# Performance work log

Measured on AMD Instinct MI355X. Metric: run time of the kernel, lower is better.

The kernel has to match this reference:

```python
import jax, jax.numpy as jnp
import numpy as np

N_HEADS = 12


def setup_inputs() -> dict:
    key = jax.random.key(0)
    ks = jax.random.split(key, 4)
    B, S, D = 2, 2048, 768
    x = jax.random.normal(ks[0], (B, S, D), dtype=jnp.float32)
    # nn.Linear-style init scale ~ 1/sqrt(D) to keep logits reasonable
    scale = 1.0 / np.sqrt(D)
    Wq = jax.random.normal(ks[1], (D, D), dtype=jnp.float32) * scale
    Wk = jax.random.normal(ks[2], (D, D), dtype=jnp.float32) * scale
    Wv = jax.random.normal(ks[3], (D, D), dtype=jnp.float32) * scale
    bq = jnp.zeros((D,), jnp.float32)
    bk = jnp.zeros((D,), jnp.float32)
    bv = jnp.zeros((D,), jnp.float32)
    mask = jnp.ones((B, S), jnp.int32)
    return {"x": x, "Wq": Wq, "bq": bq, "Wk": Wk, "bk": bk,
            "Wv": Wv, "bv": bv, "mask": mask}


def reference(x, Wq, bq, Wk, bk, Wv, bv, mask):
    B, S, D = x.shape
    H = N_HEADS
    W = D // H
    # q,k,v: (B,S,D) -> (B,H,S,W)
    def proj(Wm, bm):
        return (x @ Wm.T + bm).reshape(B, S, H, W).transpose(0, 2, 1, 3)
    q, k, v = proj(Wq, bq), proj(Wk, bk), proj(Wv, bv)
    scores = jnp.einsum("bhsw,bhtw->bhst", q, k) / jnp.sqrt(
        jnp.asarray(W, x.dtype))
    # mask: (B,S) -> broadcast over query positions; 0 -> -1e20
    scores = jnp.where(mask[:, None, None, :] == 0,
                       jnp.asarray(-1e20, scores.dtype), scores)
    attn = jax.nn.softmax(scores, axis=-1)  # (B,H,S,S)
    # dropout p=0.0 (eval) -> identity
    ctx = jnp.einsum("bhst,bhtw->bhsw", attn, v)
    hidden = ctx.transpose(0, 2, 1, 3).reshape(B, S, D)
    return hidden
```

## Files before the change

### kernel.cpp

```cpp
#include <hip/hip_runtime.h>
#include <hip/hip_bf16.h>
#include <stdint.h>


typedef __attribute__((ext_vector_type(8))) short bf16x8;
typedef __attribute__((ext_vector_type(4))) float f32x4;
typedef __attribute__((ext_vector_type(8))) unsigned short u16x8;

#define MFMA16(a, b, c) __builtin_amdgcn_mfma_f32_16x16x32_bf16((a), (b), (c), 0, 0, 0)
#define SWZ(row, colb) ((colb) ^ (((row) & 7) << 4))

__device__ __forceinline__ void gl_lds16(const void* g, void* l) {
  __builtin_amdgcn_global_load_lds(
      (__attribute__((address_space(1))) void*)const_cast<void*>(g),
      (__attribute__((address_space(3))) void*)l, 16, 0, 0);
}

__device__ __forceinline__ unsigned short f2bf(float x) {
  unsigned int v = __float_as_uint(x);
  return (unsigned short)((v + 0x7fffu + ((v >> 16) & 1u)) >> 16);
}

__global__ __launch_bounds__(256) void cvt_all(
    const float* __restrict__ x, const float* __restrict__ wq,
    const float* __restrict__ wk, const float* __restrict__ wv,
    unsigned short* __restrict__ xb, unsigned short* __restrict__ wb) {
  int i = blockIdx.x * 256 + threadIdx.x;
  const float* s;
  unsigned short* d;
  int off;
  if (i < 393216)      { s = x;  d = xb;            off = i; }
  else if (i < 466944) { s = wq; d = wb;            off = i - 393216; }
  else if (i < 540672) { s = wk; d = wb + 589824;   off = i - 466944; }
  else                 { s = wv; d = wb + 1179648;  off = i - 540672; }
  const float4* sp = (const float4*)s + (size_t)off * 2;
  float4 a = sp[0], b2 = sp[1];
  u16x8 o;
  o[0] = f2bf(a.x); o[1] = f2bf(a.y); o[2] = f2bf(a.z); o[3] = f2bf(a.w);
  o[4] = f2bf(b2.x); o[5] = f2bf(b2.y); o[6] = f2bf(b2.z); o[7] = f2bf(b2.w);
  *((u16x8*)d + off) = o;
}

__global__ __launch_bounds__(256) void proj_gemm(
    const unsigned short* __restrict__ xb, const unsigned short* __restrict__ wb,
    const float* __restrict__ bq, const float* __restrict__ bk, const float* __restrict__ bv,
    unsigned short* __restrict__ qw, unsigned short* __restrict__ kw,
    unsigned short* __restrict__ vw) {
  __shared__ unsigned short lA[128 * 64];
  __shared__ unsigned short lB[128 * 64];
  const int t = threadIdx.x, lane = t & 63, wave = t >> 6;
  const int wr = wave >> 1, wc = wave & 1;
  const int mbase = blockIdx.x * 128;
  const int wsel = blockIdx.y / 6;
  const int nbase = (blockIdx.y % 6) * 128;
  const unsigned short* wmat = wb + (size_t)wsel * 589824;

  f32x4 acc[4][4];
#pragma unroll
  for (int i = 0; i < 4; i++)
#pragma unroll
    for (int j = 0; j < 4; j++) acc[i][j] = (f32x4){0.f, 0.f, 0.f, 0.f};

  char* lAc = (char*)lA;
  char* lBc = (char*)lB;

  for (int kt = 0; kt < 768; kt += 64) {
#pragma unroll
    for (int i = 0; i < 4; i++) {
      int p = t * 16 + i * 4096;
      int row = p >> 7, colb = p & 127;
      int scol = SWZ(row, colb);
      gl_lds16((const char*)xb + ((size_t)(mbase + row) * 768 + kt) * 2 + scol, lAc + p);
      gl_lds16((const char*)wmat + ((size_t)(nbase + row) * 768 + kt) * 2 + scol, lBc + p);
    }
    __syncthreads();

    bf16x8 af[2][4], bff[2][4];
#pragma unroll
    for (int mf = 0; mf < 4; mf++) {
      int row = wr * 64 + mf * 16 + (lane & 15);
#pragma unroll
      for (int kk = 0; kk < 2; kk++)
        af[kk][mf] = *(const bf16x8*)(lAc + row * 128 + SWZ(row, kk * 64 + (lane >> 4) * 16));
    }
#pragma unroll
    for (int nf = 0; nf < 4; nf++) {
      int row = wc * 64 + nf * 16 + (lane & 15);
#pragma unroll
      for (int kk = 0; kk < 2; kk++)
        bff[kk][nf] = *(const bf16x8*)(lBc + row * 128 + SWZ(row, kk * 64 + (lane >> 4) * 16));
    }
#pragma unroll
    for (int kk = 0; kk < 2; kk++)
#pragma unroll
      for (int mf = 0; mf < 4; mf++)
#pragma unroll
        for (int nf = 0; nf < 4; nf++)
          acc[mf][nf] = MFMA16(af[kk][mf], bff[kk][nf], acc[mf][nf]);
    __syncthreads();
  }

  const float* bias = (wsel == 0) ? bq : ((wsel == 1) ? bk : bv);
  const float QSCALE = 0.125f * 1.44269504089f;
#pragma unroll
  for (int nf = 0; nf < 4; nf++) {
    int n = nbase + wc * 64 + nf * 16 + (lane & 15);
    float bv_ = bias[n];
    int h = n >> 6, wcol = n & 63;
#pragma unroll
    for (int mf = 0; mf < 4; mf++) {
#pragma unroll
      for (int r = 0; r < 4; r++) {
        int m = mbase + wr * 64 + mf * 16 + (lane >> 4) * 4 + r;
        int b = m >> 11, s = m & 2047;
        float val = acc[mf][nf][r] + bv_;
        size_t bh = (size_t)b * 12 + h;
        if (wsel == 0)
          qw[(bh * 2048 + s) * 64 + wcol] = f2bf(val * QSCALE);
        else if (wsel == 1)
          kw[(bh * 2048 + s) * 64 + wcol] = f2bf(val);
        else
          vw[(bh * 64 + wcol) * 2048 + s] = f2bf(val);
      }
    }
  }
}

__global__ __launch_bounds__(256) void attn_kernel(
    const unsigned short* __restrict__ qw, const unsigned short* __restrict__ kw,
    const unsigned short* __restrict__ vw, const int* __restrict__ mask,
    float* __restrict__ out) {
  __shared__ unsigned short lK[2][64 * 64];
  __shared__ unsigned short lV[2][64 * 64];
  __shared__ unsigned short lP[4][16 * 64];
  __shared__ unsigned long long lBal[32];
  const int t = threadIdx.x, lane = t & 63, wave = t >> 6;
  const int hi = lane >> 4, lo = lane & 15;
  const int qb = blockIdx.x, bh = blockIdx.y;
  const int b = bh / 12, h = bh - b * 12;
  char* lPc = (char*)&lP[wave][0];

  {
    const int* mb = mask + (size_t)b * 2048 + t * 8;
    int4 a0 = *(const int4*)mb;
    int4 a1 = *(const int4*)(mb + 4);
    unsigned by = (unsigned)(a0.x != 0) | ((unsigned)(a0.y != 0) << 1) |
                  ((unsigned)(a0.z != 0) << 2) | ((unsigned)(a0.w != 0) << 3) |
                  ((unsigned)(a1.x != 0) << 4) | ((unsigned)(a1.y != 0) << 5) |
                  ((unsigned)(a1.z != 0) << 6) | ((unsigned)(a1.w != 0) << 7);
    ((unsigned char*)lBal)[t] = (unsigned char)by;
  }

  bf16x8 qa0, qa1;
  {
    int qrow = qb * 64 + wave * 16 + lo;
    const char* qp = (const char*)qw + ((size_t)bh * 2048 + qrow) * 128 + hi * 16;
    qa0 = *(const bf16x8*)qp;
    qa1 = *(const bf16x8*)(qp + 64);
  }

  const char* kbaseg = (const char*)kw + (size_t)bh * 262144;
  const char* vbaseg = (const char*)vw + (size_t)bh * 262144;

  const int p0 = t * 16, p1 = t * 16 + 4096;
  const int r0 = p0 >> 7, s0 = SWZ(r0, p0 & 127);
  const int r1 = p1 >> 7, s1 = SWZ(r1, p1 & 127);

#define STAGE(IT, BUF)                                                              \
  do {                                                                              \
    int it_ = (IT);                                                                 \
    gl_lds16(kbaseg + (size_t)it_ * 8192 + r0 * 128 + s0, (char*)lK[(BUF)] + p0);   \
    gl_lds16(vbaseg + (size_t)r0 * 4096 + it_ * 128 + s0, (char*)lV[(BUF)] + p0);   \
    gl_lds16(kbaseg + (size_t)it_ * 8192 + r1 * 128 + s1, (char*)lK[(BUF)] + p1);   \
    gl_lds16(vbaseg + (size_t)r1 * 4096 + it_ * 128 + s1, (char*)lV[(BUF)] + p1);   \
  } while (0)

  f32x4 oacc[4];
#pragma unroll
  for (int nf = 0; nf < 4; nf++) oacc[nf] = (f32x4){0.f, 0.f, 0.f, 0.f};
  float lacc = 0.f;

  STAGE(0, 0);
  __syncthreads();

  for (int it = 0; it < 32; ++it) {
    STAGE((it + 1) & 31, (it + 1) & 1);
    asm volatile("s_waitcnt vmcnt(4)" ::: "memory");
    __builtin_amdgcn_s_barrier();

    const char* lKc = (const char*)lK[it & 1];
    const char* lVc = (const char*)lV[it & 1];

    f32x4 sc[4];
    __builtin_amdgcn_s_setprio(1);
#pragma unroll
    for (int nf = 0; nf < 4; nf++) {
      int row = nf * 16 + lo;
      bf16x8 kb0 = *(const bf16x8*)(lKc + row * 128 + SWZ(row, hi * 16));
      bf16x8 kb1 = *(const bf16x8*)(lKc + row * 128 + SWZ(row, 64 + hi * 16));
      f32x4 z = (f32x4){0.f, 0.f, 0.f, 0.f};
      z = MFMA16(kb0, qa0, z);
      sc[nf] = MFMA16(kb1, qa1, z);
    }
    __builtin_amdgcn_s_setprio(0);

    unsigned long long bal = lBal[it];
    if (bal != ~0ull) {
#pragma unroll
      for (int nf = 0; nf < 4; nf++)
#pragma unroll
        for (int r = 0; r < 4; r++) {
          int key = nf * 16 + hi * 4 + r;
          if (!((bal >> key) & 1)) sc[nf][r] = -30000.f;
        }
    }

#pragma unroll
    for (int nf = 0; nf < 4; nf++) {
      float e0, e1, e2, e3;
      asm("v_exp_f32 %0, %1" : "=v"(e0) : "v"(sc[nf][0]));
      asm("v_exp_f32 %0, %1" : "=v"(e1) : "v"(sc[nf][1]));
      asm("v_exp_f32 %0, %1" : "=v"(e2) : "v"(sc[nf][2]));
      asm("v_exp_f32 %0, %1" : "=v"(e3) : "v"(sc[nf][3]));
      lacc += (e0 + e1) + (e2 + e3);
      unsigned pkA, pkB;
      asm("v_cvt_pk_bf16_f32 %0, %1, %2" : "=v"(pkA) : "v"(e0), "v"(e1));
      asm("v_cvt_pk_bf16_f32 %0, %1, %2" : "=v"(pkB) : "v"(e2), "v"(e3));
      uint2 pk2;
      pk2.x = pkA;
      pk2.y = pkB;
      *(uint2*)(lPc + lo * 128 + SWZ(lo, nf * 32 + hi * 8)) = pk2;
    }

    bf16x8 pa0 = *(const bf16x8*)(lPc + lo * 128 + SWZ(lo, hi * 16));
    bf16x8 pa1 = *(const bf16x8*)(lPc + lo * 128 + SWZ(lo, 64 + hi * 16));
    __builtin_amdgcn_s_setprio(1);
#pragma unroll
    for (int nf = 0; nf < 4; nf++) {
      int row = nf * 16 + lo;
      bf16x8 vb0 = *(const bf16x8*)(lVc + row * 128 + SWZ(row, hi * 16));
      bf16x8 vb1 = *(const bf16x8*)(lVc + row * 128 + SWZ(row, 64 + hi * 16));
      oacc[nf] = MFMA16(pa0, vb0, oacc[nf]);
      oacc[nf] = MFMA16(pa1, vb1, oacc[nf]);
    }
    __builtin_amdgcn_s_setprio(0);
    __builtin_amdgcn_s_barrier();
  }
  asm volatile("s_waitcnt vmcnt(0)" ::: "memory");

  lacc += __shfl_xor(lacc, 16);
  lacc += __shfl_xor(lacc, 32);
#pragma unroll
  for (int r = 0; r < 4; r++) {
    int q = hi * 4 + r;
    float linv = 1.0f / __shfl(lacc, q);
    int s = qb * 64 + wave * 16 + q;
    float* op = out + ((size_t)b * 2048 + s) * 768 + h * 64;
#pragma unroll
    for (int nf = 0; nf < 4; nf++) op[nf * 16 + lo] = oacc[nf][r] * linv;
  }
#undef STAGE
}

extern "C" void kernel_launch(void* const* d_in, const int* in_sizes, int n_in,
                              void* d_out, int out_size, void* d_ws, size_t ws_size,
                              hipStream_t stream) {
  (void)in_sizes; (void)n_in; (void)out_size; (void)ws_size;
  const float* x  = (const float*)d_in[0];
  const float* Wq = (const float*)d_in[1];
  const float* bq = (const float*)d_in[2];
  const float* Wk = (const float*)d_in[3];
  const float* bk = (const float*)d_in[4];
  const float* Wv = (const float*)d_in[5];
  const float* bv = (const float*)d_in[6];
  const int* mask = (const int*)d_in[7];
  float* out = (float*)d_out;

  char* ws = (char*)d_ws;
  unsigned short* xb = (unsigned short*)(ws);
  unsigned short* wb = (unsigned short*)(ws + 6291456);
  unsigned short* qw = (unsigned short*)(ws + 9830400);
  unsigned short* kw = (unsigned short*)(ws + 16121856);
  unsigned short* vw = (unsigned short*)(ws + 22413312);

  cvt_all<<<2400, 256, 0, stream>>>(x, Wq, Wk, Wv, xb, wb);
  proj_gemm<<<dim3(32, 18), 256, 0, stream>>>(xb, wb, bq, bk, bv, qw, kw, vw);
  attn_kernel<<<dim3(32, 24), 256, 0, stream>>>(qw, kw, vw, mask, out);
}
```

Baseline: 94.69 us.

## Switch attention to 32x32 MFMA with key-split waves and register P transpose

Rewrites the attention inner loop to use 32x32x16 bf16 MFMAs, splitting each 64x64 tile across waves as 2 query-halves times 2 key-halves. Softmax probabilities are moved into A-operand layout with v_permlane32_swap instead of a round trip through LDS. Partial outputs and row sums from the two key-halves are reduced through shared memory at the end. The V projection epilogue is also transposed so that V stores are contiguous along the sequence. The change adds a final cross-wave reduction and sync, and sets launch bounds for 4 blocks per CU.

```diff
diff --git a/kernel.cpp b/kernel.cpp
--- a/kernel.cpp
+++ b/kernel.cpp
@@ -5,10 +5,17 @@
 
 typedef __attribute__((ext_vector_type(8))) short bf16x8;
 typedef __attribute__((ext_vector_type(4))) float f32x4;
+typedef __attribute__((ext_vector_type(16))) float f32x16;
 typedef __attribute__((ext_vector_type(8))) unsigned short u16x8;
 
 #define MFMA16(a, b, c) __builtin_amdgcn_mfma_f32_16x16x32_bf16((a), (b), (c), 0, 0, 0)
+#define MFMA32(a, b, c) __builtin_amdgcn_mfma_f32_32x32x16_bf16((a), (b), (c), 0, 0, 0)
 #define SWZ(row, colb) ((colb) ^ (((row) & 7) << 4))
+
+union U32x4BF {
+  unsigned u[4];
+  bf16x8 v;
+};
 
 __device__ __forceinline__ void gl_lds16(const void* g, void* l) {
   __builtin_amdgcn_global_load_lds(
@@ -90,55 +97,78 @@
       for (int kk = 0; kk < 2; kk++)
         bff[kk][nf] = *(const bf16x8*)(lBc + row * 128 + SWZ(row, kk * 64 + (lane >> 4) * 16));
     }
-#pragma unroll
-    for (int kk = 0; kk < 2; kk++)
-#pragma unroll
-      for (int mf = 0; mf < 4; mf++)
-#pragma unroll
-        for (int nf = 0; nf < 4; nf++)
-          acc[mf][nf] = MFMA16(af[kk][mf], bff[kk][nf], acc[mf][nf]);
+    if (wsel == 2) {
+#pragma unroll
+      for (int kk = 0; kk < 2; kk++)
+#pragma unroll
+        for (int mf = 0; mf < 4; mf++)
+#pragma unroll
+          for (int nf = 0; nf < 4; nf++)
+            acc[mf][nf] = MFMA16(bff[kk][nf], af[kk][mf], acc[mf][nf]);
+    } else {
+#pragma unroll
+      for (int kk = 0; kk < 2; kk++)
+#pragma unroll
+        for (int mf = 0; mf < 4; mf++)
+#pragma unroll
+          for (int nf = 0; nf < 4; nf++)
+            acc[mf][nf] = MFMA16(af[kk][mf], bff[kk][nf], acc[mf][nf]);
+    }
     __syncthreads();
   }
 
-  const float* bias = (wsel == 0) ? bq : ((wsel == 1) ? bk : bv);
   const float QSCALE = 0.125f * 1.44269504089f;
-#pragma unroll
-  for (int nf = 0; nf < 4; nf++) {
-    int n = nbase + wc * 64 + nf * 16 + (lane & 15);
-    float bv_ = bias[n];
-    int h = n >> 6, wcol = n & 63;
-#pragma unroll
-    for (int mf = 0; mf < 4; mf++) {
-#pragma unroll
-      for (int r = 0; r < 4; r++) {
-        int m = mbase + wr * 64 + mf * 16 + (lane >> 4) * 4 + r;
-        int b = m >> 11, s = m & 2047;
-        float val = acc[mf][nf][r] + bv_;
-        size_t bh = (size_t)b * 12 + h;
-        if (wsel == 0)
-          qw[(bh * 2048 + s) * 64 + wcol] = f2bf(val * QSCALE);
-        else if (wsel == 1)
-          kw[(bh * 2048 + s) * 64 + wcol] = f2bf(val);
-        else
-          vw[(bh * 64 + wcol) * 2048 + s] = f2bf(val);
-      }
-    }
-  }
-}
-
-__global__ __launch_bounds__(256) void attn_kernel(
+  if (wsel == 2) {
+#pragma unroll
+    for (int nf = 0; nf < 4; nf++) {
+#pragma unroll
+      for (int mf = 0; mf < 4; mf++) {
+#pragma unroll
+        for (int r = 0; r < 4; r++) {
+          int n = nbase + wc * 64 + nf * 16 + (lane >> 4) * 4 + r;
+          int m = mbase + wr * 64 + mf * 16 + (lane & 15);
+          int b_ = m >> 11, s = m & 2047;
+          int h = n >> 6, wcol = n & 63;
+          float val = acc[mf][nf][r] + bv[n];
+          vw[(((size_t)b_ * 12 + h) * 64 + wcol) * 2048 + s] = f2bf(val);
+        }
+      }
+    }
+  } else {
+    const float* bias = (wsel == 0) ? bq : bk;
+#pragma unroll
+    for (int nf = 0; nf < 4; nf++) {
+      int n = nbase + wc * 64 + nf * 16 + (lane & 15);
+      float bv_ = bias[n];
+      int h = n >> 6, wcol = n & 63;
+#pragma unroll
+      for (int mf = 0; mf < 4; mf++) {
+#pragma unroll
+        for (int r = 0; r < 4; r++) {
+          int m = mbase + wr * 64 + mf * 16 + (lane >> 4) * 4 + r;
+          int b_ = m >> 11, s = m & 2047;
+          float val = acc[mf][nf][r] + bv_;
+          size_t bhh = (size_t)b_ * 12 + h;
+          if (wsel == 0)
+            qw[(bhh * 2048 + s) * 64 + wcol] = f2bf(val * QSCALE);
+          else
+            kw[(bhh * 2048 + s) * 64 + wcol] = f2bf(val);
+        }
+      }
+    }
+  }
+}
+
+__global__ __launch_bounds__(256, 4) void attn_kernel(
     const unsigned short* __restrict__ qw, const unsigned short* __restrict__ kw,
     const unsigned short* __restrict__ vw, const int* __restrict__ mask,
     float* __restrict__ out) {
-  __shared__ unsigned short lK[2][64 * 64];
-  __shared__ unsigned short lV[2][64 * 64];
-  __shared__ unsigned short lP[4][16 * 64];
-  __shared__ unsigned long long lBal[32];
+  __shared__ __align__(16) char smem[33536];
   const int t = threadIdx.x, lane = t & 63, wave = t >> 6;
-  const int hi = lane >> 4, lo = lane & 15;
+  const int wq = wave >> 1, wk = wave & 1;
+  const int l31 = lane & 31, hl = lane >> 5;
   const int qb = blockIdx.x, bh = blockIdx.y;
-  const int b = bh / 12, h = bh - b * 12;
-  char* lPc = (char*)&lP[wave][0];
+  const int b = bh / 12, hh = bh - b * 12;
 
   {
     const int* mb = mask + (size_t)b * 2048 + t * 8;
@@ -148,15 +178,15 @@
                   ((unsigned)(a0.z != 0) << 2) | ((unsigned)(a0.w != 0) << 3) |
                   ((unsigned)(a1.x != 0) << 4) | ((unsigned)(a1.y != 0) << 5) |
                   ((unsigned)(a1.z != 0) << 6) | ((unsigned)(a1.w != 0) << 7);
-    ((unsigned char*)lBal)[t] = (unsigned char)by;
-  }
-
-  bf16x8 qa0, qa1;
+    smem[32768 + t] = (char)by;
+  }
+
+  bf16x8 qv[4];
   {
-    int qrow = qb * 64 + wave * 16 + lo;
-    const char* qp = (const char*)qw + ((size_t)bh * 2048 + qrow) * 128 + hi * 16;
-    qa0 = *(const bf16x8*)qp;
-    qa1 = *(const bf16x8*)(qp + 64);
+    int qrow = qb * 64 + wq * 32 + l31;
+    const char* qp = (const char*)qw + ((size_t)bh * 2048 + qrow) * 128 + hl * 16;
+#pragma unroll
+    for (int s = 0; s < 4; s++) qv[s] = *(const bf16x8*)(qp + s * 32);
   }
 
   const char* kbaseg = (const char*)kw + (size_t)bh * 262144;
@@ -166,98 +196,136 @@
   const int r0 = p0 >> 7, s0 = SWZ(r0, p0 & 127);
   const int r1 = p1 >> 7, s1 = SWZ(r1, p1 & 127);
 
-#define STAGE(IT, BUF)                                                              \
-  do {                                                                              \
-    int it_ = (IT);                                                                 \
-    gl_lds16(kbaseg + (size_t)it_ * 8192 + r0 * 128 + s0, (char*)lK[(BUF)] + p0);   \
-    gl_lds16(vbaseg + (size_t)r0 * 4096 + it_ * 128 + s0, (char*)lV[(BUF)] + p0);   \
-    gl_lds16(kbaseg + (size_t)it_ * 8192 + r1 * 128 + s1, (char*)lK[(BUF)] + p1);   \
-    gl_lds16(vbaseg + (size_t)r1 * 4096 + it_ * 128 + s1, (char*)lV[(BUF)] + p1);   \
+#define STAGE(IT, BUF)                                                                   \
+  do {                                                                                   \
+    int it_ = (IT);                                                                      \
+    gl_lds16(kbaseg + (size_t)it_ * 8192 + r0 * 128 + s0, smem + (BUF) * 8192 + p0);     \
+    gl_lds16(vbaseg + (size_t)r0 * 4096 + it_ * 128 + s0, smem + 16384 + (BUF) * 8192 + p0); \
+    gl_lds16(kbaseg + (size_t)it_ * 8192 + r1 * 128 + s1, smem + (BUF) * 8192 + p1);     \
+    gl_lds16(vbaseg + (size_t)r1 * 4096 + it_ * 128 + s1, smem + 16384 + (BUF) * 8192 + p1); \
   } while (0)
 
-  f32x4 oacc[4];
-#pragma unroll
-  for (int nf = 0; nf < 4; nf++) oacc[nf] = (f32x4){0.f, 0.f, 0.f, 0.f};
+  f32x16 oacc[2];
+#pragma unroll
+  for (int wh = 0; wh < 2; wh++)
+#pragma unroll
+    for (int g = 0; g < 16; g++) oacc[wh][g] = 0.f;
   float lacc = 0.f;
 
   STAGE(0, 0);
   __syncthreads();
 
   for (int it = 0; it < 32; ++it) {
-    STAGE((it + 1) & 31, (it + 1) & 1);
-    asm volatile("s_waitcnt vmcnt(4)" ::: "memory");
+    if (it < 31) {
+      STAGE(it + 1, (it + 1) & 1);
+      asm volatile("s_waitcnt vmcnt(4)" ::: "memory");
+    } else {
+      asm volatile("s_waitcnt vmcnt(0)" ::: "memory");
+    }
     __builtin_amdgcn_s_barrier();
 
-    const char* lKc = (const char*)lK[it & 1];
-    const char* lVc = (const char*)lV[it & 1];
-
-    f32x4 sc[4];
+    const char* lKc = smem + (it & 1) * 8192;
+    const char* lVc = smem + 16384 + (it & 1) * 8192;
+
+    f32x16 sc;
+#pragma unroll
+    for (int g = 0; g < 16; g++) sc[g] = 0.f;
+    const int krow = wk * 32 + l31;
     __builtin_amdgcn_s_setprio(1);
 #pragma unroll
-    for (int nf = 0; nf < 4; nf++) {
-      int row = nf * 16 + lo;
-      bf16x8 kb0 = *(const bf16x8*)(lKc + row * 128 + SWZ(row, hi * 16));
-      bf16x8 kb1 = *(const bf16x8*)(lKc + row * 128 + SWZ(row, 64 + hi * 16));
-      f32x4 z = (f32x4){0.f, 0.f, 0.f, 0.f};
-      z = MFMA16(kb0, qa0, z);
-      sc[nf] = MFMA16(kb1, qa1, z);
+    for (int s = 0; s < 4; s++) {
+      bf16x8 kf = *(const bf16x8*)(lKc + krow * 128 + SWZ(krow, s * 32 + hl * 16));
+      sc = MFMA32(kf, qv[s], sc);
     }
     __builtin_amdgcn_s_setprio(0);
 
-    unsigned long long bal = lBal[it];
+    unsigned long long bal = *(const unsigned long long*)(smem + 32768 + it * 8);
     if (bal != ~0ull) {
 #pragma unroll
-      for (int nf = 0; nf < 4; nf++)
-#pragma unroll
-        for (int r = 0; r < 4; r++) {
-          int key = nf * 16 + hi * 4 + r;
-          if (!((bal >> key) & 1)) sc[nf][r] = -30000.f;
-        }
-    }
-
-#pragma unroll
-    for (int nf = 0; nf < 4; nf++) {
-      float e0, e1, e2, e3;
-      asm("v_exp_f32 %0, %1" : "=v"(e0) : "v"(sc[nf][0]));
-      asm("v_exp_f32 %0, %1" : "=v"(e1) : "v"(sc[nf][1]));
-      asm("v_exp_f32 %0, %1" : "=v"(e2) : "v"(sc[nf][2]));
-      asm("v_exp_f32 %0, %1" : "=v"(e3) : "v"(sc[nf][3]));
-      lacc += (e0 + e1) + (e2 + e3);
-      unsigned pkA, pkB;
-      asm("v_cvt_pk_bf16_f32 %0, %1, %2" : "=v"(pkA) : "v"(e0), "v"(e1));
-      asm("v_cvt_pk_bf16_f32 %0, %1, %2" : "=v"(pkB) : "v"(e2), "v"(e3));
-      uint2 pk2;
-      pk2.x = pkA;
-      pk2.y = pkB;
-      *(uint2*)(lPc + lo * 128 + SWZ(lo, nf * 32 + hi * 8)) = pk2;
-    }
-
-    bf16x8 pa0 = *(const bf16x8*)(lPc + lo * 128 + SWZ(lo, hi * 16));
-    bf16x8 pa1 = *(const bf16x8*)(lPc + lo * 128 + SWZ(lo, 64 + hi * 16));
+      for (int g = 0; g < 16; g++) {
+        int key = wk * 32 + 4 * hl + (g & 3) + 8 * (g >> 2);
+        if (!((bal >> key) & 1)) sc[g] = -30000.f;
+      }
+    }
+
+    float e[16];
+#pragma unroll
+    for (int g = 0; g < 16; g++)
+      asm("v_exp_f32 %0, %1" : "=v"(e[g]) : "v"(sc[g]));
+    lacc += (((e[0] + e[1]) + (e[2] + e[3])) + ((e[4] + e[5]) + (e[6] + e[7]))) +
+            (((e[8] + e[9]) + (e[10] + e[11])) + ((e[12] + e[13]) + (e[14] + e[15])));
+    unsigned pk[4][2];
+#pragma unroll
+    for (int m = 0; m < 4; m++) {
+      asm("v_cvt_pk_bf16_f32 %0, %1, %2" : "=v"(pk[m][0]) : "v"(e[4 * m]), "v"(e[4 * m + 1]));
+      asm("v_cvt_pk_bf16_f32 %0, %1, %2" : "=v"(pk[m][1]) : "v"(e[4 * m + 2]), "v"(e[4 * m + 3]));
+    }
+    U32x4BF apv[2];
+#pragma unroll
+    for (int sp = 0; sp < 2; sp++)
+#pragma unroll
+      for (int cp = 0; cp < 2; cp++) {
+        unsigned xx = pk[2 * sp][cp], yy = pk[2 * sp + 1][cp];
+        asm("v_permlane32_swap_b32 %0, %1" : "+v"(xx), "+v"(yy));
+        apv[sp].u[cp] = xx;
+        apv[sp].u[2 + cp] = yy;
+      }
+
     __builtin_amdgcn_s_setprio(1);
 #pragma unroll
-    for (int nf = 0; nf < 4; nf++) {
-      int row = nf * 16 + lo;
-      bf16x8 vb0 = *(const bf16x8*)(lVc + row * 128 + SWZ(row, hi * 16));
-      bf16x8 vb1 = *(const bf16x8*)(lVc + row * 128 + SWZ(row, 64 + hi * 16));
-      oacc[nf] = MFMA16(pa0, vb0, oacc[nf]);
-      oacc[nf] = MFMA16(pa1, vb1, oacc[nf]);
+    for (int wh = 0; wh < 2; wh++) {
+      int vrow = wh * 32 + l31;
+#pragma unroll
+      for (int sp = 0; sp < 2; sp++) {
+        bf16x8 vf = *(const bf16x8*)(lVc + vrow * 128 + SWZ(vrow, wk * 64 + sp * 32 + hl * 16));
+        oacc[wh] = MFMA32(apv[sp].v, vf, oacc[wh]);
+      }
     }
     __builtin_amdgcn_s_setprio(0);
     __builtin_amdgcn_s_barrier();
   }
-  asm volatile("s_waitcnt vmcnt(0)" ::: "memory");
-
-  lacc += __shfl_xor(lacc, 16);
+
   lacc += __shfl_xor(lacc, 32);
-#pragma unroll
-  for (int r = 0; r < 4; r++) {
-    int q = hi * 4 + r;
-    float linv = 1.0f / __shfl(lacc, q);
-    int s = qb * 64 + wave * 16 + q;
-    float* op = out + ((size_t)b * 2048 + s) * 768 + h * 64;
-#pragma unroll
-    for (int nf = 0; nf < 4; nf++) op[nf * 16 + lo] = oacc[nf][r] * linv;
+  if (lane < 32)
+    *(float*)(smem + 33024 + (wk * 64 + wq * 32 + l31) * 4) = lacc;
+  if (wk == 1) {
+#pragma unroll
+    for (int wh = 0; wh < 2; wh++) {
+      int vrow = wh * 32 + l31;
+#pragma unroll
+      for (int m = 0; m < 4; m++) {
+        f32x4 part = (f32x4){oacc[wh][4 * m], oacc[wh][4 * m + 1],
+                             oacc[wh][4 * m + 2], oacc[wh][4 * m + 3]};
+        *(f32x4*)(smem + wq * 8192 + vrow * 128 + SWZ(vrow, hl * 16 + m * 32)) = part;
+      }
+    }
+  }
+  __syncthreads();
+  if (wk == 0) {
+    float linv[16];
+#pragma unroll
+    for (int g = 0; g < 16; g++) {
+      int qrow = 4 * hl + (g & 3) + 8 * (g >> 2);
+      float l0 = *(const float*)(smem + 33024 + (wq * 32 + qrow) * 4);
+      float l1 = *(const float*)(smem + 33024 + (64 + wq * 32 + qrow) * 4);
+      linv[g] = __builtin_amdgcn_rcpf(l0 + l1);
+    }
+#pragma unroll
+    for (int wh = 0; wh < 2; wh++) {
+      int vrow = wh * 32 + l31;
+#pragma unroll
+      for (int m = 0; m < 4; m++) {
+        f32x4 part = *(const f32x4*)(smem + wq * 8192 + vrow * 128 + SWZ(vrow, hl * 16 + m * 32));
+#pragma unroll
+        for (int r = 0; r < 4; r++) {
+          int g = 4 * m + r;
+          int qrow = 4 * hl + r + 8 * m;
+          float val = (oacc[wh][g] + part[r]) * linv[g];
+          out[((size_t)b * 2048 + qb * 64 + wq * 32 + qrow) * 768 + hh * 64 + wh * 32 + l31] =
+              val;
+        }
+      }
+    }
   }
 #undef STAGE
 }
```

After: 88.39 us. 6.6% less time.
